# Performance work log

Measured on AMD Instinct MI355X. Metric: run time of the kernel, lower is better.

Reference implementation:

```python
import jax, jax.numpy as jnp
import numpy as np

B, C, O, H, W = 4, 64, 64, 64, 64  # inch=outch=64 (view() in source requires outch==inch)


def setup_inputs() -> dict:
    key = jax.random.key(0)
    ks = jax.random.split(key, 9)
    s = lambda k, shape: jax.random.normal(k, shape, jnp.float32) * 0.05
    return {
        "x": jax.random.normal(ks[0], (B, C, H, W), jnp.float32),
        "w_theta": s(ks[1], (O, C)), "b_theta": s(ks[2], (O,)),
        "w_phi": s(ks[3], (O, C)), "b_phi": s(ks[4], (O,)),
        "w_g": s(ks[5], (O, C)), "b_g": s(ks[6], (O,)),
        "w_out": s(ks[7], (C, O)), "b_out": s(ks[8], (C,)),
        "bn_gamma": jnp.ones((C,), jnp.float32),
        "bn_beta": jnp.zeros((C,), jnp.float32),
    }


def reference(x, w_theta, b_theta, w_phi, b_phi, w_g, b_g, w_out, b_out, bn_gamma, bn_beta):
    b, c, h, w = x.shape
    n = h * w
    conv1x1 = lambda wt, bt: jnp.einsum('bchw,oc->bohw', x, wt) + bt[None, :, None, None]
    theta = conv1x1(w_theta, b_theta).reshape(b, -1, n)  # [B,O,N]
    phi = conv1x1(w_phi, b_phi).reshape(b, -1, n)        # [B,O,N]
    g = conv1x1(w_g, b_g).reshape(b, -1, n)              # [B,O,N]
    # scores[b,n,m] = sum_o theta[b,o,n] * phi[b,o,m]  (theta permuted to [B,N,O] in torch)
    attn = jax.nn.softmax(jnp.einsum('bon,bom->bnm', theta, phi), axis=-1)  # [B,N,N]
    # dropout is identity in eval mode
    y = jnp.einsum('bnm,bom->bon', attn, g).reshape(b, -1, h, w)  # [B,O,H,W]
    z = jnp.einsum('bohw,co->bchw', y, w_out) + b_out[None, :, None, None]
    z = jax.nn.relu(z)
    eps = 1e-5  # eval-mode BatchNorm2d: running_mean=0, running_var=1
    z = z * (bn_gamma * jax.lax.rsqrt(jnp.float32(1.0 + eps)))[None, :, None, None] \
        + bn_beta[None, :, None, None]
    return x + z
```

## Files before the change

kernel.cpp:

```cpp
#include <hip/hip_runtime.h>

typedef __attribute__((ext_vector_type(4))) float f32x4;
typedef __attribute__((ext_vector_type(16))) float f32x16;
typedef __attribute__((ext_vector_type(8))) short bf16x8;
typedef unsigned short u16;
typedef unsigned int u32;

constexpr int NN = 4096;

__device__ __forceinline__ u16 f2bf(float f){
  u32 u = __builtin_bit_cast(u32, f);
  u += 0x7FFFu + ((u >> 16) & 1u);
  return (u16)(u >> 16);
}
__device__ __forceinline__ u32 cvtpk(float lo, float hi){
  u32 r;
  asm("v_cvt_pk_bf16_f32 %0, %1, %2" : "=v"(r) : "v"(lo), "v"(hi));
  return r;
}
__device__ __forceinline__ float fexp2(float x){
  float r;
  asm("v_exp_f32 %0, %1" : "=v"(r) : "v"(x));
  return r;
}
__device__ __forceinline__ void async16(void* lds, const void* g){
  __builtin_amdgcn_global_load_lds((const __attribute__((address_space(1))) void*)g,
                                   (__attribute__((address_space(3))) void*)lds,
                                   16, 0, 0);
}

__global__ __launch_bounds__(512) void proj_kernel(
    const float* __restrict__ x,
    const float* __restrict__ wth, const float* __restrict__ bth,
    const float* __restrict__ wph, const float* __restrict__ bph,
    const float* __restrict__ wg,  const float* __restrict__ bg,
    u16* __restrict__ theta_t, u16* __restrict__ phi_t, u16* __restrict__ gbuf)
{
  __shared__ float Wsm[3 * 4096];
  __shared__ float Bsm[3 * 64];

  const int t = threadIdx.x;
#pragma unroll
  for (int i = 0; i < 6; ++i){
    const int idx = i * 512 + t;
    const float4 v = (idx < 1024) ? ((const float4*)wth)[idx]
                   : (idx < 2048) ? ((const float4*)wph)[idx - 1024]
                                  : ((const float4*)wg)[idx - 2048];
    ((float4*)Wsm)[idx] = v;
  }
  if (t < 192) Bsm[t] = (t < 64) ? bth[t] : (t < 128) ? bph[t - 64] : bg[t - 128];

  const int b = blockIdx.x >> 6;
  const int n = (blockIdx.x & 63) * 64 + (t & 63);
  const int w = __builtin_amdgcn_readfirstlane(t >> 6);
  const int ob = w * 8;

  const float* xb = x + ((size_t)b * 64) * NN + n;
  float xr[64];
#pragma unroll
  for (int c = 0; c < 64; ++c) xr[c] = xb[(size_t)c * NN];

  __syncthreads();

  for (int mat = 0; mat < 3; ++mat){
    const float* Wm = Wsm + mat * 4096 + ob * 64;
    float acc[8];
#pragma unroll
    for (int oo = 0; oo < 8; ++oo) acc[oo] = Bsm[mat * 64 + ob + oo];
#pragma unroll
    for (int c4 = 0; c4 < 16; ++c4)
#pragma unroll
      for (int oo = 0; oo < 8; ++oo){
        const float4 wv = *(const float4*)&Wm[oo * 64 + c4 * 4];
        acc[oo] = fmaf(wv.x, xr[4 * c4],     acc[oo]);
        acc[oo] = fmaf(wv.y, xr[4 * c4 + 1], acc[oo]);
        acc[oo] = fmaf(wv.z, xr[4 * c4 + 2], acc[oo]);
        acc[oo] = fmaf(wv.w, xr[4 * c4 + 3], acc[oo]);
      }
    if (mat == 0){
#pragma unroll
      for (int oo = 0; oo < 8; ++oo) acc[oo] *= 1.44269504088896340736f;
    }
    if (mat < 2){
      uint4 pk;
      pk.x = cvtpk(acc[0], acc[1]); pk.y = cvtpk(acc[2], acc[3]);
      pk.z = cvtpk(acc[4], acc[5]); pk.w = cvtpk(acc[6], acc[7]);
      u16* base = (mat == 0) ? theta_t : phi_t;
      *(uint4*)(base + ((size_t)(b * NN + n)) * 64 + ob) = pk;
    } else {
#pragma unroll
      for (int oo = 0; oo < 8; ++oo)
        gbuf[((size_t)(b * 64 + ob + oo)) * NN + n] = f2bf(acc[oo]);
    }
  }
}

template<int TPB>
__global__ __launch_bounds__(512, 4) void attn_kernel(
    const u16* __restrict__ theta_t, const u16* __restrict__ phi_t,
    const u16* __restrict__ gbuf,
    u16* __restrict__ y_part, float* __restrict__ l_part)
{
  __shared__ u16 phi_sm[3][64 * 64];
  __shared__ u16 g_sm[3][64 * 64];

  const int j   = blockIdx.x;
  const int cpx = gridDim.x >> 3;
  const int lb  = (j & 7) * cpx + (j >> 3);

  const int ms  = lb >> 6;
  const int pr  = lb & 63;
  const int b   = pr >> 4;
  const int n0  = (pr & 15) * 256;

  const int tid = threadIdx.x;
  const int w   = __builtin_amdgcn_readfirstlane(tid >> 6);
  const int l   = tid & 63;
  const int cc  = l & 31;
  const int h   = l >> 5;
  const int sw  = (cc & 7) << 4;
  const int rb  = cc * 128;

  const u16* thb = theta_t + (size_t)b * NN * 64;

  bf16x8 tf[4];
#pragma unroll
  for (int ks = 0; ks < 4; ++ks)
    tf[ks] = *(const bf16x8*)(thb + (size_t)(n0 + w * 32 + cc) * 64 + ks * 16 + h * 8);

  const int m0 = ms * TPB;
  const int r8 = l >> 3;
  const int c8 = l & 7;
  const u16* phi_src = phi_t + (size_t)b * NN * 64
                     + (size_t)(m0 * 64 + w * 8 + r8) * 64 + (c8 ^ r8) * 8;
  const u16* g_src   = gbuf + (size_t)b * 64 * NN
                     + (size_t)(w * 8 + r8) * NN + m0 * 64 + (c8 ^ r8) * 8;

  f32x16 yacc0, yacc1;
#pragma unroll
  for (int i = 0; i < 16; ++i){ yacc0[i] = 0.f; yacc1[i] = 0.f; }
  float lacc = 0.f;

  async16(&phi_sm[0][w * 512], phi_src);
  async16(&g_sm[0][w * 512],   g_src);
  phi_src += 4096; g_src += 64;
  async16(&phi_sm[1][w * 512], phi_src);
  async16(&g_sm[1][w * 512],   g_src);
  phi_src += 4096; g_src += 64;

#pragma unroll
  for (int it = 0; it < TPB; ++it){
    const int cur = it % 3;
    if (it < TPB - 1)
      asm volatile("s_waitcnt vmcnt(2)" ::: "memory");
    else
      asm volatile("s_waitcnt vmcnt(0)" ::: "memory");
    asm volatile("" ::: "memory");
    __builtin_amdgcn_s_barrier();
    asm volatile("" ::: "memory");
    if (it + 2 < TPB){
      async16(&phi_sm[(it + 2) % 3][w * 512], phi_src);
      async16(&g_sm[(it + 2) % 3][w * 512],   g_src);
      phi_src += 4096; g_src += 64;
    }

    const char* phiB = (const char*)&phi_sm[cur][0];
    const char* gB   = (const char*)&g_sm[cur][0];

#pragma unroll
    for (int tt = 0; tt < 2; ++tt){
      __builtin_amdgcn_s_setprio(1);
      f32x16 p;
#pragma unroll
      for (int i = 0; i < 16; ++i) p[i] = 0.f;
#pragma unroll
      for (int ks = 0; ks < 4; ++ks)
        p = __builtin_amdgcn_mfma_f32_32x32x16_bf16(
              *(const bf16x8*)(phiB + tt * 4096 + rb + ((ks * 32 + h * 16) ^ sw)),
              tf[ks], p, 0, 0, 0);
      __builtin_amdgcn_s_setprio(0);

      u32 wpk[4][2];
#pragma unroll
      for (int rq = 0; rq < 4; ++rq){
        const float e0 = fexp2(p[4 * rq + 0]), e1 = fexp2(p[4 * rq + 1]);
        const float e2 = fexp2(p[4 * rq + 2]), e3 = fexp2(p[4 * rq + 3]);
        lacc += (e0 + e1) + (e2 + e3);
        wpk[rq][0] = cvtpk(e0, e1);
        wpk[rq][1] = cvtpk(e2, e3);
      }

      __builtin_amdgcn_s_setprio(1);
#pragma unroll
      for (int par = 0; par < 2; ++par){
        u32 A0 = wpk[2 * par][0],     A1 = wpk[2 * par][1];
        u32 B0 = wpk[2 * par + 1][0], B1 = wpk[2 * par + 1][1];
        asm("v_permlane32_swap_b32 %0, %1" : "+v"(A0), "+v"(B0));
        asm("v_permlane32_swap_b32 %0, %1" : "+v"(A1), "+v"(B1));
        union { u32 u[4]; bf16x8 v; } pw;
        pw.u[0] = A0; pw.u[1] = A1; pw.u[2] = B0; pw.u[3] = B1;
        const int s   = tt * 2 + par;
        const int gof = (s * 32 + h * 16) ^ sw;
        yacc0 = __builtin_amdgcn_mfma_f32_32x32x16_bf16(
                  pw.v, *(const bf16x8*)(gB + rb + gof), yacc0, 0, 0, 0);
        yacc1 = __builtin_amdgcn_mfma_f32_32x32x16_bf16(
                  pw.v, *(const bf16x8*)(gB + 4096 + rb + gof), yacc1, 0, 0, 0);
      }
      __builtin_amdgcn_s_setprio(0);
    }
  }

  {
    u32 la = __builtin_bit_cast(u32, lacc), lb2 = la;
    asm("v_permlane32_swap_b32 %0, %1" : "+v"(la), "+v"(lb2));
    const float ltot = __builtin_bit_cast(float, la) + __builtin_bit_cast(float, lb2);
    if (l < 32)
      l_part[(size_t)(ms * 4 + b) * NN + n0 + w * 32 + cc] = ltot;
  }

  u16* yp = y_part + ((size_t)(ms * 4 + b) * NN + n0 + w * 32) * 64 + cc;
#pragma unroll
  for (int r = 0; r < 16; ++r){
    const int nl = (r & 3) + 8 * (r >> 2) + 4 * h;
    yp[(size_t)nl * 64]      = f2bf(yacc0[r]);
    yp[(size_t)nl * 64 + 32] = f2bf(yacc1[r]);
  }
}

__global__ __launch_bounds__(256) void combine_kernel(
    const u16* __restrict__ y_part, const float* __restrict__ l_part,
    const float* __restrict__ x,
    const float* __restrict__ w_out, const float* __restrict__ b_out,
    const float* __restrict__ bn_gamma, const float* __restrict__ bn_beta,
    float* __restrict__ out, int S)
{
  __shared__ u16 y_sm[32 * 64];
  __shared__ float inv_sm[32];

  const int cb   = blockIdx.x;
  const int b    = cb >> 7;
  const int nin  = (cb & 127) * 32;
  const int t    = threadIdx.x;
  const int row  = t >> 3;
  const int ch   = t & 7;

  float s[8] = {0.f,0.f,0.f,0.f,0.f,0.f,0.f,0.f};
  for (int ms = 0; ms < S; ++ms){
    const u16* src = y_part + ((size_t)(ms * 4 + b) * NN + nin + row) * 64 + ch * 8;
    const uint4 v = *(const uint4*)src;
    const u32 ww[4] = {v.x, v.y, v.z, v.w};
#pragma unroll
    for (int i = 0; i < 4; ++i){
      s[2 * i]     += __builtin_bit_cast(float, ww[i] << 16);
      s[2 * i + 1] += __builtin_bit_cast(float, ww[i] & 0xFFFF0000u);
    }
  }
  if (t < 32){
    float ls = 0.f;
    for (int ms = 0; ms < S; ++ms)
      ls += l_part[(size_t)(ms * 4 + b) * NN + nin + t];
    inv_sm[t] = 1.0f / ls;
  }
  __syncthreads();

  {
    const float inv = inv_sm[row];
    uint4 pk;
    pk.x = cvtpk(s[0] * inv, s[1] * inv);
    pk.y = cvtpk(s[2] * inv, s[3] * inv);
    pk.z = cvtpk(s[4] * inv, s[5] * inv);
    pk.w = cvtpk(s[6] * inv, s[7] * inv);
    *(uint4*)((char*)y_sm + ((row * 128 + ch * 16) ^ ((row & 7) << 4))) = pk;
  }
  __syncthreads();

  const int w   = __builtin_amdgcn_readfirstlane(t >> 6);
  const int l   = t & 63;
  const int q   = l & 15;
  const int gg  = l >> 4;
  const int swz = (q & 7) << 4;

  bf16x8 wf[2];
#pragma unroll
  for (int ks = 0; ks < 2; ++ks){
    bf16x8 v;
#pragma unroll
    for (int jj = 0; jj < 8; ++jj)
      v[jj] = (short)f2bf(w_out[(w * 16 + q) * 64 + ks * 32 + gg * 8 + jj]);
    wf[ks] = v;
  }
  f32x4 zacc[2];
  zacc[0] = (f32x4){0.f, 0.f, 0.f, 0.f};
  zacc[1] = (f32x4){0.f, 0.f, 0.f, 0.f};
#pragma unroll
  for (int ks = 0; ks < 2; ++ks)
#pragma unroll
    for (int ns = 0; ns < 2; ++ns){
      const int off = (((ns * 16 + q) * 128) + ks * 64 + gg * 16) ^ swz;
      const bf16x8 yf = *(const bf16x8*)((const char*)y_sm + off);
      zacc[ns] = __builtin_amdgcn_mfma_f32_16x16x32_bf16(wf[ks], yf, zacc[ns], 0, 0, 0);
    }

  float bo[4], sc_[4], bb_[4];
#pragma unroll
  for (int r = 0; r < 4; ++r){
    const int c = w * 16 + gg * 4 + r;
    bo[r]  = b_out[c];
    sc_[r] = bn_gamma[c] * 0.99999500003749969f;
    bb_[r] = bn_beta[c];
  }
#pragma unroll
  for (int ns = 0; ns < 2; ++ns)
#pragma unroll
    for (int r = 0; r < 4; ++r){
      const int c  = w * 16 + gg * 4 + r;
      const int ng = nin + ns * 16 + q;
      const size_t idx = ((size_t)(b * 64 + c)) * NN + ng;
      float z = zacc[ns][r] + bo[r];
      z = fmaxf(z, 0.0f);
      z = z * sc_[r] + bb_[r];
      out[idx] = x[idx] + z;
    }
}

extern "C" void kernel_launch(void* const* d_in, const int* in_sizes, int n_in,
                              void* d_out, int out_size, void* d_ws, size_t ws_size,
                              hipStream_t stream)
{
  (void)in_sizes; (void)n_in; (void)out_size;
  const float* x        = (const float*)d_in[0];
  const float* w_theta  = (const float*)d_in[1];
  const float* b_theta  = (const float*)d_in[2];
  const float* w_phi    = (const float*)d_in[3];
  const float* b_phi    = (const float*)d_in[4];
  const float* w_g      = (const float*)d_in[5];
  const float* b_g      = (const float*)d_in[6];
  const float* w_out    = (const float*)d_in[7];
  const float* b_out    = (const float*)d_in[8];
  const float* bn_gamma = (const float*)d_in[9];
  const float* bn_beta  = (const float*)d_in[10];
  float* out = (float*)d_out;

  u16* theta_t = (u16*)d_ws;
  u16* phi_t   = theta_t + (size_t)4 * NN * 64;
  u16* gbuf    = phi_t   + (size_t)4 * NN * 64;
  char* after  = (char*)(gbuf + (size_t)4 * NN * 64);
  const size_t used = (size_t)(after - (char*)d_ws);
  const size_t perS = (size_t)4 * NN * 64 * 2 + (size_t)4 * NN * 4;

  int S = 1;
  if      (ws_size >= used + 8 * perS) S = 8;
  else if (ws_size >= used + 4 * perS) S = 4;
  else if (ws_size >= used + 2 * perS) S = 2;
  u16*   y_part = (u16*)after;
  float* l_part = (float*)(y_part + (size_t)S * 4 * NN * 64);

  proj_kernel<<<256, 512, 0, stream>>>(x, w_theta, b_theta, w_phi, b_phi,
                                       w_g, b_g, theta_t, phi_t, gbuf);
  if (S == 8)
    attn_kernel<8><<<512, 512, 0, stream>>>(theta_t, phi_t, gbuf, y_part, l_part);
  else if (S == 4)
    attn_kernel<16><<<256, 512, 0, stream>>>(theta_t, phi_t, gbuf, y_part, l_part);
  else if (S == 2)
    attn_kernel<32><<<128, 512, 0, stream>>>(theta_t, phi_t, gbuf, y_part, l_part);
  else
    attn_kernel<64><<<64, 512, 0, stream>>>(theta_t, phi_t, gbuf, y_part, l_part);
  combine_kernel<<<512, 256, 0, stream>>>(y_part, l_part, x, w_out, b_out,
                                          bn_gamma, bn_beta, out, S);
}
```

Measured before the change: 48.75 us.

## Double query rows per wave in attention kernel to reuse phi/g tiles

Each wave now computes scores and PV accumulation for two 32-row query tiles, sharing each loaded phi and g LDS fragment across both. The grid is halved and launch bounds are relaxed to 2 blocks per CU to fit the doubled accumulators. This cuts LDS reads and global phi/g loads per unit of work. The trade is higher register pressure and fewer blocks for latency hiding and load balancing.

```diff
diff --git a/kernel.cpp b/kernel.cpp
--- a/kernel.cpp
+++ b/kernel.cpp
@@ -96,7 +96,7 @@
 }
 
 template<int TPB>
-__global__ __launch_bounds__(512, 4) void attn_kernel(
+__global__ __launch_bounds__(512, 2) void attn_kernel(
     const u16* __restrict__ theta_t, const u16* __restrict__ phi_t,
     const u16* __restrict__ gbuf,
     u16* __restrict__ y_part, float* __restrict__ l_part)
@@ -108,10 +108,10 @@
   const int cpx = gridDim.x >> 3;
   const int lb  = (j & 7) * cpx + (j >> 3);
 
-  const int ms  = lb >> 6;
-  const int pr  = lb & 63;
-  const int b   = pr >> 4;
-  const int n0  = (pr & 15) * 256;
+  const int ms  = lb >> 5;
+  const int pr  = lb & 31;
+  const int b   = pr >> 3;
+  const int n0  = (pr & 7) * 512;
 
   const int tid = threadIdx.x;
   const int w   = __builtin_amdgcn_readfirstlane(tid >> 6);
@@ -123,10 +123,12 @@
 
   const u16* thb = theta_t + (size_t)b * NN * 64;
 
-  bf16x8 tf[4];
-#pragma unroll
-  for (int ks = 0; ks < 4; ++ks)
-    tf[ks] = *(const bf16x8*)(thb + (size_t)(n0 + w * 32 + cc) * 64 + ks * 16 + h * 8);
+  bf16x8 tf0[4], tf1[4];
+#pragma unroll
+  for (int ks = 0; ks < 4; ++ks){
+    tf0[ks] = *(const bf16x8*)(thb + (size_t)(n0 + w * 64 + cc) * 64 + ks * 16 + h * 8);
+    tf1[ks] = *(const bf16x8*)(thb + (size_t)(n0 + w * 64 + 32 + cc) * 64 + ks * 16 + h * 8);
+  }
 
   const int m0 = ms * TPB;
   const int r8 = l >> 3;
@@ -136,10 +138,12 @@
   const u16* g_src   = gbuf + (size_t)b * 64 * NN
                      + (size_t)(w * 8 + r8) * NN + m0 * 64 + (c8 ^ r8) * 8;
 
-  f32x16 yacc0, yacc1;
-#pragma unroll
-  for (int i = 0; i < 16; ++i){ yacc0[i] = 0.f; yacc1[i] = 0.f; }
-  float lacc = 0.f;
+  f32x16 yacc00, yacc01, yacc10, yacc11;
+#pragma unroll
+  for (int i = 0; i < 16; ++i){
+    yacc00[i] = 0.f; yacc01[i] = 0.f; yacc10[i] = 0.f; yacc11[i] = 0.f;
+  }
+  float lacc0 = 0.f, lacc1 = 0.f;
 
   async16(&phi_sm[0][w * 512], phi_src);
   async16(&g_sm[0][w * 512],   g_src);
@@ -170,60 +174,83 @@
 #pragma unroll
     for (int tt = 0; tt < 2; ++tt){
       __builtin_amdgcn_s_setprio(1);
-      f32x16 p;
-#pragma unroll
-      for (int i = 0; i < 16; ++i) p[i] = 0.f;
-#pragma unroll
-      for (int ks = 0; ks < 4; ++ks)
-        p = __builtin_amdgcn_mfma_f32_32x32x16_bf16(
-              *(const bf16x8*)(phiB + tt * 4096 + rb + ((ks * 32 + h * 16) ^ sw)),
-              tf[ks], p, 0, 0, 0);
+      f32x16 p0, p1;
+#pragma unroll
+      for (int i = 0; i < 16; ++i){ p0[i] = 0.f; p1[i] = 0.f; }
+#pragma unroll
+      for (int ks = 0; ks < 4; ++ks){
+        const bf16x8 pf = *(const bf16x8*)(phiB + tt * 4096 + rb + ((ks * 32 + h * 16) ^ sw));
+        p0 = __builtin_amdgcn_mfma_f32_32x32x16_bf16(pf, tf0[ks], p0, 0, 0, 0);
+        p1 = __builtin_amdgcn_mfma_f32_32x32x16_bf16(pf, tf1[ks], p1, 0, 0, 0);
+      }
       __builtin_amdgcn_s_setprio(0);
 
-      u32 wpk[4][2];
+      u32 wpk0[4][2], wpk1[4][2];
 #pragma unroll
       for (int rq = 0; rq < 4; ++rq){
-        const float e0 = fexp2(p[4 * rq + 0]), e1 = fexp2(p[4 * rq + 1]);
-        const float e2 = fexp2(p[4 * rq + 2]), e3 = fexp2(p[4 * rq + 3]);
-        lacc += (e0 + e1) + (e2 + e3);
-        wpk[rq][0] = cvtpk(e0, e1);
-        wpk[rq][1] = cvtpk(e2, e3);
+        float e0 = fexp2(p0[4 * rq + 0]), e1 = fexp2(p0[4 * rq + 1]);
+        float e2 = fexp2(p0[4 * rq + 2]), e3 = fexp2(p0[4 * rq + 3]);
+        lacc0 += (e0 + e1) + (e2 + e3);
+        wpk0[rq][0] = cvtpk(e0, e1);
+        wpk0[rq][1] = cvtpk(e2, e3);
+        e0 = fexp2(p1[4 * rq + 0]); e1 = fexp2(p1[4 * rq + 1]);
+        e2 = fexp2(p1[4 * rq + 2]); e3 = fexp2(p1[4 * rq + 3]);
+        lacc1 += (e0 + e1) + (e2 + e3);
+        wpk1[rq][0] = cvtpk(e0, e1);
+        wpk1[rq][1] = cvtpk(e2, e3);
       }
 
       __builtin_amdgcn_s_setprio(1);
 #pragma unroll
       for (int par = 0; par < 2; ++par){
-        u32 A0 = wpk[2 * par][0],     A1 = wpk[2 * par][1];
-        u32 B0 = wpk[2 * par + 1][0], B1 = wpk[2 * par + 1][1];
+        u32 A0 = wpk0[2 * par][0],     A1 = wpk0[2 * par][1];
+        u32 B0 = wpk0[2 * par + 1][0], B1 = wpk0[2 * par + 1][1];
         asm("v_permlane32_swap_b32 %0, %1" : "+v"(A0), "+v"(B0));
         asm("v_permlane32_swap_b32 %0, %1" : "+v"(A1), "+v"(B1));
-        union { u32 u[4]; bf16x8 v; } pw;
-        pw.u[0] = A0; pw.u[1] = A1; pw.u[2] = B0; pw.u[3] = B1;
+        union { u32 u[4]; bf16x8 v; } pw0;
+        pw0.u[0] = A0; pw0.u[1] = A1; pw0.u[2] = B0; pw0.u[3] = B1;
+        u32 C0 = wpk1[2 * par][0],     C1 = wpk1[2 * par][1];
+        u32 D0 = wpk1[2 * par + 1][0], D1 = wpk1[2 * par + 1][1];
+        asm("v_permlane32_swap_b32 %0, %1" : "+v"(C0), "+v"(D0));
+        asm("v_permlane32_swap_b32 %0, %1" : "+v"(C1), "+v"(D1));
+        union { u32 u[4]; bf16x8 v; } pw1;
+        pw1.u[0] = C0; pw1.u[1] = C1; pw1.u[2] = D0; pw1.u[3] = D1;
+
         const int s   = tt * 2 + par;
         const int gof = (s * 32 + h * 16) ^ sw;
-        yacc0 = __builtin_amdgcn_mfma_f32_32x32x16_bf16(
-                  pw.v, *(const bf16x8*)(gB + rb + gof), yacc0, 0, 0, 0);
-        yacc1 = __builtin_amdgcn_mfma_f32_32x32x16_bf16(
-                  pw.v, *(const bf16x8*)(gB + 4096 + rb + gof), yacc1, 0, 0, 0);
+        const bf16x8 g0 = *(const bf16x8*)(gB + rb + gof);
+        const bf16x8 g1 = *(const bf16x8*)(gB + 4096 + rb + gof);
+        yacc00 = __builtin_amdgcn_mfma_f32_32x32x16_bf16(pw0.v, g0, yacc00, 0, 0, 0);
+        yacc01 = __builtin_amdgcn_mfma_f32_32x32x16_bf16(pw0.v, g1, yacc01, 0, 0, 0);
+        yacc10 = __builtin_amdgcn_mfma_f32_32x32x16_bf16(pw1.v, g0, yacc10, 0, 0, 0);
+        yacc11 = __builtin_amdgcn_mfma_f32_32x32x16_bf16(pw1.v, g1, yacc11, 0, 0, 0);
       }
       __builtin_amdgcn_s_setprio(0);
     }
   }
 
   {
-    u32 la = __builtin_bit_cast(u32, lacc), lb2 = la;
+    u32 la = __builtin_bit_cast(u32, lacc0), lb2 = la;
     asm("v_permlane32_swap_b32 %0, %1" : "+v"(la), "+v"(lb2));
-    const float ltot = __builtin_bit_cast(float, la) + __builtin_bit_cast(float, lb2);
-    if (l < 32)
-      l_part[(size_t)(ms * 4 + b) * NN + n0 + w * 32 + cc] = ltot;
-  }
-
-  u16* yp = y_part + ((size_t)(ms * 4 + b) * NN + n0 + w * 32) * 64 + cc;
+    const float lt0 = __builtin_bit_cast(float, la) + __builtin_bit_cast(float, lb2);
+    u32 lc = __builtin_bit_cast(u32, lacc1), ld = lc;
+    asm("v_permlane32_swap_b32 %0, %1" : "+v"(lc), "+v"(ld));
+    const float lt1 = __builtin_bit_cast(float, lc) + __builtin_bit_cast(float, ld);
+    if (l < 32){
+      l_part[(size_t)(ms * 4 + b) * NN + n0 + w * 64 + cc]      = lt0;
+      l_part[(size_t)(ms * 4 + b) * NN + n0 + w * 64 + 32 + cc] = lt1;
+    }
+  }
+
+  u16* yp0 = y_part + ((size_t)(ms * 4 + b) * NN + n0 + w * 64) * 64 + cc;
+  u16* yp1 = y_part + ((size_t)(ms * 4 + b) * NN + n0 + w * 64 + 32) * 64 + cc;
 #pragma unroll
   for (int r = 0; r < 16; ++r){
     const int nl = (r & 3) + 8 * (r >> 2) + 4 * h;
-    yp[(size_t)nl * 64]      = f2bf(yacc0[r]);
-    yp[(size_t)nl * 64 + 32] = f2bf(yacc1[r]);
+    yp0[(size_t)nl * 64]      = f2bf(yacc00[r]);
+    yp0[(size_t)nl * 64 + 32] = f2bf(yacc01[r]);
+    yp1[(size_t)nl * 64]      = f2bf(yacc10[r]);
+    yp1[(size_t)nl * 64 + 32] = f2bf(yacc11[r]);
   }
 }
 
@@ -358,13 +385,13 @@
   proj_kernel<<<256, 512, 0, stream>>>(x, w_theta, b_theta, w_phi, b_phi,
                                        w_g, b_g, theta_t, phi_t, gbuf);
   if (S == 8)
-    attn_kernel<8><<<512, 512, 0, stream>>>(theta_t, phi_t, gbuf, y_part, l_part);
+    attn_kernel<8><<<256, 512, 0, stream>>>(theta_t, phi_t, gbuf, y_part, l_part);
   else if (S == 4)
-    attn_kernel<16><<<256, 512, 0, stream>>>(theta_t, phi_t, gbuf, y_part, l_part);
+    attn_kernel<16><<<128, 512, 0, stream>>>(theta_t, phi_t, gbuf, y_part, l_part);
   else if (S == 2)
-    attn_kernel<32><<<128, 512, 0, stream>>>(theta_t, phi_t, gbuf, y_part, l_part);
+    attn_kernel<32><<<64, 512, 0, stream>>>(theta_t, phi_t, gbuf, y_part, l_part);
   else
-    attn_kernel<64><<<64, 512, 0, stream>>>(theta_t, phi_t, gbuf, y_part, l_part);
+    attn_kernel<64><<<32, 512, 0, stream>>>(theta_t, phi_t, gbuf, y_part, l_part);
   combine_kernel<<<512, 256, 0, stream>>>(y_part, l_part, x, w_out, b_out,
                                           bn_gamma, bn_beta, out, S);
 }
```

Measured after the change: 47.51 us. 1.03x faster.
